# Optimization experiments

Measured on AMD Instinct MI355X. Metric: run time of the kernel, lower is better.

Reference implementation:

```python
import jax, jax.numpy as jnp
import numpy as np

N_NODES = 50000


def setup_inputs() -> dict:
    key = jax.random.key(0)
    k1, k2, k3, k4, k5 = jax.random.split(key, 5)
    x = jax.random.normal(k1, (N_NODES, 128), dtype=jnp.float32)
    edge_index = jax.random.randint(k2, (1600000, 2), 0, N_NODES, dtype=jnp.int64)
    # learned params for the concrete combine: out = agg @ W_neigh + self @ W_self + b
    W_neigh = jax.random.normal(k3, (128, 128), dtype=jnp.float32) * (1.0 / np.sqrt(128))
    W_self = jax.random.normal(k4, (128, 128), dtype=jnp.float32) * (1.0 / np.sqrt(128))
    b = jax.random.normal(k5, (128,), dtype=jnp.float32) * 0.01
    return {"x": x, "edge_index": edge_index, "W_neigh": W_neigh, "W_self": W_self, "b": b}


def reference(x, edge_index, W_neigh, W_self, b):
    n = x.shape[0]
    src = edge_index[:, 0]
    dst = edge_index[:, 1]
    # undirected: each edge (i,j) sends x[j] -> i and x[i] -> j
    agg_sum = jax.ops.segment_sum(x[dst], src, num_segments=n)
    agg_sum = agg_sum + jax.ops.segment_sum(x[src], dst, num_segments=n)
    ones = jnp.ones((edge_index.shape[0],), dtype=x.dtype)
    deg = jax.ops.segment_sum(ones, src, num_segments=n)
    deg = deg + jax.ops.segment_sum(ones, dst, num_segments=n)
    agg_mean = agg_sum / jnp.maximum(deg, 1.0)[:, None]  # mean aggregate
    # combine(agg, self)
    return agg_mean @ W_neigh + x @ W_self + b
```

## Files before the change

kernel.cpp:

```cpp
#include <hip/hip_runtime.h>
#include <hip/hip_fp16.h>


constexpr int DIM    = 128;
constexpr int NBMAX  = 512;
constexpr int EPB    = 4096;
constexpr int CAP    = 9216;

typedef _Float16 half8 __attribute__((ext_vector_type(8)));
typedef __attribute__((ext_vector_type(4))) float f32x4;

__device__ __forceinline__ unsigned hadd2u(unsigned a, unsigned b) {
    __half2 ha = *reinterpret_cast<__half2*>(&a);
    __half2 hb = *reinterpret_cast<__half2*>(&b);
    __half2 r  = __hadd2(ha, hb);
    return *reinterpret_cast<unsigned*>(&r);
}
__device__ __forceinline__ unsigned hmul2u(unsigned a, __half2 s) {
    __half2 ha = *reinterpret_cast<__half2*>(&a);
    __half2 r  = __hmul2(ha, s);
    return *reinterpret_cast<unsigned*>(&r);
}
__device__ __forceinline__ unsigned packf16(float x, float y) {
    __half2 h = __floats2half2_rn(x, y);
    return *reinterpret_cast<unsigned*>(&h);
}

__global__ __launch_bounds__(256) void k_prep(
    const float* __restrict__ Wn, const float* __restrict__ Ws,
    const float* __restrict__ x,
    unsigned short* __restrict__ Bp, int* __restrict__ bucket_cur,
    unsigned* __restrict__ abf, int nb, int n_nodes)
{
    int i = blockIdx.x * 256 + threadIdx.x;
    if (i < nb) bucket_cur[i] = i * CAP;
    if (i < 8 * 128 * 4 * 8) {
        int j    = i & 7;
        int quad = (i >> 3) & 3;
        int n    = (i >> 5) & 127;
        int kb   = i >> 12;
        int k = kb * 32 + quad * 8 + j;
        float v = (k < 128) ? Wn[k * 128 + n] : Ws[(k - 128) * 128 + n];
        __half h = __float2half_rn(v);
        Bp[i] = *reinterpret_cast<unsigned short*>(&h);
    }
    if (i < n_nodes * 64) {
        int n = i >> 6;
        int u = i & 63;
        float2 f = ((const float2*)(x + (size_t)n * DIM))[u];
        abf[(size_t)n * 128 + 64 + u] = packf16(f.x, f.y);
    }
}

__global__ __launch_bounds__(512) void k_bin(
    const int* __restrict__ edge, int* __restrict__ bucket_cur,
    unsigned* __restrict__ entries, int n_edges, int nb)
{
    __shared__ int lh[8][NBMAX];
    __shared__ int Lb[NBMAX];
    __shared__ int gb[NBMAX];
    __shared__ int sc[NBMAX];
    __shared__ unsigned sorted[2 * EPB];

    int t = threadIdx.x;
    int w = t >> 6;
    for (int i = t; i < 8 * NBMAX; i += 512) ((int*)lh)[i] = 0;
    __syncthreads();

    int e0 = blockIdx.x * EPB;
    int2 ev[8];
    #pragma unroll
    for (int k = 0; k < 8; k++) {
        int idx = e0 + k * 512 + t;
        if (idx < n_edges) {
            ev[k] = ((const int2*)edge)[idx];
            atomicAdd(&lh[w][ev[k].x >> 7], 1);
            atomicAdd(&lh[w][ev[k].y >> 7], 1);
        } else {
            ev[k].x = -1;
        }
    }
    __syncthreads();

    {
        int s = 0;
        #pragma unroll
        for (int ww = 0; ww < 8; ww++) s += lh[ww][t];
        sc[t] = s;
    }
    __syncthreads();
    for (int d = 1; d < 512; d <<= 1) {
        int v = (t >= d) ? sc[t - d] : 0;
        __syncthreads();
        if (t >= d) sc[t] += v;
        __syncthreads();
    }
    if (t < nb) {
        int tot = 0;
        #pragma unroll
        for (int ww = 0; ww < 8; ww++) tot += lh[ww][t];
        int L = sc[t] - tot;
        Lb[t] = L;
        gb[t] = tot ? atomicAdd(&bucket_cur[t], tot) : 0;
        int run = L;
        #pragma unroll
        for (int ww = 0; ww < 8; ww++) { int c = lh[ww][t]; lh[ww][t] = run; run += c; }
    }
    __syncthreads();

    #pragma unroll
    for (int k = 0; k < 8; k++) {
        int a = ev[k].x;
        if (a < 0) continue;
        int b = ev[k].y;
        int sa = atomicAdd(&lh[w][a >> 7], 1);
        sorted[sa] = ((unsigned)a << 16) | (unsigned)b;
        int sb = atomicAdd(&lh[w][b >> 7], 1);
        sorted[sb] = ((unsigned)b << 16) | (unsigned)a;
    }
    __syncthreads();

    int cntb = sc[511];
    for (int p = t; p < cntb; p += 512) {
        unsigned e = sorted[p];
        int bk = (int)(e >> 23);
        entries[gb[bk] + p - Lb[bk]] = e;
    }
}

__global__ __launch_bounds__(512) void k_csort(
    const unsigned* __restrict__ entries, const int* __restrict__ bucket_cur,
    unsigned* __restrict__ offsets, int* __restrict__ degs,
    unsigned short* __restrict__ nbr, int n_nodes)
{
    int b    = blockIdx.x;
    int base = b * CAP;
    int cnt  = bucket_cur[b] - base;
    __shared__ int lh[8][128];
    __shared__ int scn[128];
    int t = threadIdx.x;
    int w = t >> 6;
    for (int i = t; i < 8 * 128; i += 512) ((int*)lh)[i] = 0;
    __syncthreads();
    for (int i = t; i < cnt; i += 512)
        atomicAdd(&lh[w][(entries[base + i] >> 16) & 127], 1);
    __syncthreads();
    int tot = 0;
    if (t < 128) {
        #pragma unroll
        for (int ww = 0; ww < 8; ww++) tot += lh[ww][t];
        scn[t] = tot;
    }
    __syncthreads();
    for (int d = 1; d < 128; d <<= 1) {
        int u = (t >= d && t < 128) ? scn[t - d] : 0;
        __syncthreads();
        if (t >= d && t < 128) scn[t] += u;
        __syncthreads();
    }
    if (t < 128) {
        int excl = scn[t] - tot;
        int node = (b << 7) + t;
        if (node < n_nodes) {
            offsets[node] = (unsigned)(base + excl);
            degs[node]    = tot;
        }
        int run = excl;
        #pragma unroll
        for (int ww = 0; ww < 8; ww++) { int c = lh[ww][t]; lh[ww][t] = run; run += c; }
    }
    __syncthreads();
    for (int i = t; i < cnt; i += 512) {
        unsigned e = entries[base + i];
        int slot = atomicAdd(&lh[w][(e >> 16) & 127], 1);
        nbr[base + slot] = (unsigned short)(e & 0xFFFFu);
    }
}

__global__ __launch_bounds__(256) void k_gather(
    const unsigned* __restrict__ offsets,
    const int* __restrict__ degs,
    const unsigned short* __restrict__ nbr,
    unsigned* __restrict__ abf, int n_nodes)
{
    int node = blockIdx.x * 4 + (threadIdx.x >> 6);
    if (node >= n_nodes) return;
    int lane = threadIdx.x & 63;
    int grp  = lane >> 4;
    int u    = lane & 15;
    const uint4* xr = (const uint4*)abf;
    int base = (int)offsets[node];
    int deg  = degs[node];
    int end  = base + deg;

    unsigned p0[4], p1[4], p2[4], p3[4];
    #pragma unroll
    for (int d = 0; d < 4; d++) { p0[d] = 0u; p1[d] = 0u; p2[d] = 0u; p3[d] = 0u; }

    int i = base + grp;
    for (; i + 12 < end; i += 16) {
        int v0 = nbr[i];
        int v1 = nbr[i + 4];
        int v2 = nbr[i + 8];
        int v3 = nbr[i + 12];
        uint4 w0 = xr[v0 * 32 + 16 + u];
        uint4 w1 = xr[v1 * 32 + 16 + u];
        uint4 w2 = xr[v2 * 32 + 16 + u];
        uint4 w3 = xr[v3 * 32 + 16 + u];
        p0[0] = hadd2u(p0[0], w0.x); p1[0] = hadd2u(p1[0], w0.y);
        p2[0] = hadd2u(p2[0], w0.z); p3[0] = hadd2u(p3[0], w0.w);
        p0[1] = hadd2u(p0[1], w1.x); p1[1] = hadd2u(p1[1], w1.y);
        p2[1] = hadd2u(p2[1], w1.z); p3[1] = hadd2u(p3[1], w1.w);
        p0[2] = hadd2u(p0[2], w2.x); p1[2] = hadd2u(p1[2], w2.y);
        p2[2] = hadd2u(p2[2], w2.z); p3[2] = hadd2u(p3[2], w2.w);
        p0[3] = hadd2u(p0[3], w3.x); p1[3] = hadd2u(p1[3], w3.y);
        p2[3] = hadd2u(p2[3], w3.z); p3[3] = hadd2u(p3[3], w3.w);
    }
    for (; i < end; i += 4) {
        int v0 = nbr[i];
        uint4 w0 = xr[v0 * 32 + 16 + u];
        p0[0] = hadd2u(p0[0], w0.x); p1[0] = hadd2u(p1[0], w0.y);
        p2[0] = hadd2u(p2[0], w0.z); p3[0] = hadd2u(p3[0], w0.w);
    }

    unsigned s0 = hadd2u(hadd2u(p0[0], p0[1]), hadd2u(p0[2], p0[3]));
    unsigned s1 = hadd2u(hadd2u(p1[0], p1[1]), hadd2u(p1[2], p1[3]));
    unsigned s2 = hadd2u(hadd2u(p2[0], p2[1]), hadd2u(p2[2], p2[3]));
    unsigned s3 = hadd2u(hadd2u(p3[0], p3[1]), hadd2u(p3[2], p3[3]));

    #pragma unroll
    for (int off = 16; off < 64; off <<= 1) {
        s0 = hadd2u(s0, (unsigned)__shfl_xor((int)s0, off));
        s1 = hadd2u(s1, (unsigned)__shfl_xor((int)s1, off));
        s2 = hadd2u(s2, (unsigned)__shfl_xor((int)s2, off));
        s3 = hadd2u(s3, (unsigned)__shfl_xor((int)s3, off));
    }

    if (grp == 0) {
        float inv = 1.0f / fmaxf((float)deg, 1.0f);
        __half2 iv = __float2half2_rn(inv);
        uint4 o;
        o.x = hmul2u(s0, iv);
        o.y = hmul2u(s1, iv);
        o.z = hmul2u(s2, iv);
        o.w = hmul2u(s3, iv);
        ((uint4*)(abf + (size_t)node * 128))[u] = o;
    }
}

__global__ __launch_bounds__(256) void k_mfma_gemm(
    const unsigned short* __restrict__ abf,
    const unsigned short* __restrict__ Bp,
    const float* __restrict__ bias,
    float* __restrict__ out, int n_nodes)
{
    int wave = threadIdx.x >> 6;
    int lane = threadIdx.x & 63;
    int quad = lane >> 4;
    int l16  = lane & 15;
    int row0 = blockIdx.x * 64 + wave * 16;

    int arow = min(row0 + l16, n_nodes - 1);
    const unsigned short* arp = abf + (size_t)arow * 256 + quad * 8;
    half8 afrag[8];
    #pragma unroll
    for (int kb = 0; kb < 8; kb++)
        afrag[kb] = *((const half8*)(arp + kb * 32));

    f32x4 acc[8];
    #pragma unroll
    for (int f = 0; f < 8; f++) acc[f] = (f32x4){0.f, 0.f, 0.f, 0.f};

    #pragma unroll
    for (int kb = 0; kb < 8; kb++) {
        #pragma unroll
        for (int f = 0; f < 8; f++) {
            int n = f * 16 + l16;
            half8 bfrag = *((const half8*)(Bp + (((size_t)kb * 128 + n) * 4 + quad) * 8));
            acc[f] = __builtin_amdgcn_mfma_f32_16x16x32_f16(afrag[kb], bfrag, acc[f], 0, 0, 0);
        }
    }

    #pragma unroll
    for (int f = 0; f < 8; f++) {
        float bv = bias[f * 16 + l16];
        #pragma unroll
        for (int r = 0; r < 4; r++) {
            int row = row0 + quad * 4 + r;
            if (row < n_nodes)
                out[(size_t)row * DIM + f * 16 + l16] = acc[f][r] + bv;
        }
    }
}

extern "C" void kernel_launch(void* const* d_in, const int* in_sizes, int n_in,
                              void* d_out, int out_size, void* d_ws, size_t ws_size,
                              hipStream_t stream) {
    const float* x    = (const float*)d_in[0];
    const int*   edge = (const int*)  d_in[1];
    const float* Wn   = (const float*)d_in[2];
    const float* Ws   = (const float*)d_in[3];
    const float* b    = (const float*)d_in[4];
    float* out = (float*)d_out;

    const int n_nodes = in_sizes[0] / DIM;
    const int n_edges = in_sizes[1] / 2;
    const int nb = (n_nodes + 127) >> 7;

    unsigned* entries      = (unsigned*)d_ws;
    unsigned short* nbr    = (unsigned short*)(entries + (size_t)nb * CAP);
    unsigned* offsets      = (unsigned*)(nbr + (size_t)nb * CAP);
    int* degs              = (int*)(offsets + n_nodes);
    int* bucket_cur        = degs + n_nodes;
    unsigned short* Bp     = (unsigned short*)((((size_t)(bucket_cur + nb)) + 63) & ~(size_t)63);
    unsigned* abf          = (unsigned*)d_out;

    const int nprep = n_nodes * 64;
    k_prep<<<(nprep + 255) / 256, 256, 0, stream>>>(Wn, Ws, x, Bp, bucket_cur,
                                                    abf, nb, n_nodes);

    const int bb = (n_edges + EPB - 1) / EPB;
    k_bin<<<bb, 512, 0, stream>>>(edge, bucket_cur, entries, n_edges, nb);
    k_csort<<<nb, 512, 0, stream>>>(entries, bucket_cur, offsets, degs, nbr, n_nodes);

    k_gather<<<(n_nodes + 3) / 4, 256, 0, stream>>>(offsets, degs, nbr, abf, n_nodes);

    const int mb = (n_nodes + 63) / 64;
    k_mfma_gemm<<<mb, 256, 0, stream>>>((const unsigned short*)abf, Bp, b,
                                        out, n_nodes);
}
```

Before: 233.9 us.

## Fuse neighbor gather-mean into MFMA GEMM via shared-memory A tile

Merges the gather/mean kernel and the MFMA GEMM into one kernel. Each block aggregates 64 nodes into an LDS tile (padded stride 68), then loads the A fragments from LDS for the neighbor half and from a compact fp16 x copy for the self half. This removes the round trip of the aggregated fp16 rows through global memory and one launch. The x copy now uses a dense 64-word stride in workspace, which halves the gather footprint. The trade-off is lower parallelism: only 782 blocks of 4 waves, each wave processing 16 nodes serially, which may hurt latency hiding for the random gathers.

Result: slower. 267.4 us (+14.3%).

```diff
diff --git a/kernel.cpp b/kernel.cpp
--- a/kernel.cpp
+++ b/kernel.cpp
@@ -30,7 +30,7 @@
     const float* __restrict__ Wn, const float* __restrict__ Ws,
     const float* __restrict__ x,
     unsigned short* __restrict__ Bp, int* __restrict__ bucket_cur,
-    unsigned* __restrict__ abf, int nb, int n_nodes)
+    unsigned* __restrict__ xt, int nb, int n_nodes)
 {
     int i = blockIdx.x * 256 + threadIdx.x;
     if (i < nb) bucket_cur[i] = i * CAP;
@@ -48,7 +48,7 @@
         int n = i >> 6;
         int u = i & 63;
         float2 f = ((const float2*)(x + (size_t)n * DIM))[u];
-        abf[(size_t)n * 128 + 64 + u] = packf16(f.x, f.y);
+        xt[(size_t)n * 64 + u] = packf16(f.x, f.y);
     }
 }
 
@@ -177,95 +177,102 @@
     }
 }
 
-__global__ __launch_bounds__(256) void k_gather(
+__global__ __launch_bounds__(256) void k_gg(
     const unsigned* __restrict__ offsets,
     const int* __restrict__ degs,
     const unsigned short* __restrict__ nbr,
-    unsigned* __restrict__ abf, int n_nodes)
-{
-    int node = blockIdx.x * 4 + (threadIdx.x >> 6);
-    if (node >= n_nodes) return;
-    int lane = threadIdx.x & 63;
-    int grp  = lane >> 4;
-    int u    = lane & 15;
-    const uint4* xr = (const uint4*)abf;
-    int base = (int)offsets[node];
-    int deg  = degs[node];
-    int end  = base + deg;
-
-    unsigned p0[4], p1[4], p2[4], p3[4];
-    #pragma unroll
-    for (int d = 0; d < 4; d++) { p0[d] = 0u; p1[d] = 0u; p2[d] = 0u; p3[d] = 0u; }
-
-    int i = base + grp;
-    for (; i + 12 < end; i += 16) {
-        int v0 = nbr[i];
-        int v1 = nbr[i + 4];
-        int v2 = nbr[i + 8];
-        int v3 = nbr[i + 12];
-        uint4 w0 = xr[v0 * 32 + 16 + u];
-        uint4 w1 = xr[v1 * 32 + 16 + u];
-        uint4 w2 = xr[v2 * 32 + 16 + u];
-        uint4 w3 = xr[v3 * 32 + 16 + u];
-        p0[0] = hadd2u(p0[0], w0.x); p1[0] = hadd2u(p1[0], w0.y);
-        p2[0] = hadd2u(p2[0], w0.z); p3[0] = hadd2u(p3[0], w0.w);
-        p0[1] = hadd2u(p0[1], w1.x); p1[1] = hadd2u(p1[1], w1.y);
-        p2[1] = hadd2u(p2[1], w1.z); p3[1] = hadd2u(p3[1], w1.w);
-        p0[2] = hadd2u(p0[2], w2.x); p1[2] = hadd2u(p1[2], w2.y);
-        p2[2] = hadd2u(p2[2], w2.z); p3[2] = hadd2u(p3[2], w2.w);
-        p0[3] = hadd2u(p0[3], w3.x); p1[3] = hadd2u(p1[3], w3.y);
-        p2[3] = hadd2u(p2[3], w3.z); p3[3] = hadd2u(p3[3], w3.w);
-    }
-    for (; i < end; i += 4) {
-        int v0 = nbr[i];
-        uint4 w0 = xr[v0 * 32 + 16 + u];
-        p0[0] = hadd2u(p0[0], w0.x); p1[0] = hadd2u(p1[0], w0.y);
-        p2[0] = hadd2u(p2[0], w0.z); p3[0] = hadd2u(p3[0], w0.w);
-    }
-
-    unsigned s0 = hadd2u(hadd2u(p0[0], p0[1]), hadd2u(p0[2], p0[3]));
-    unsigned s1 = hadd2u(hadd2u(p1[0], p1[1]), hadd2u(p1[2], p1[3]));
-    unsigned s2 = hadd2u(hadd2u(p2[0], p2[1]), hadd2u(p2[2], p2[3]));
-    unsigned s3 = hadd2u(hadd2u(p3[0], p3[1]), hadd2u(p3[2], p3[3]));
-
-    #pragma unroll
-    for (int off = 16; off < 64; off <<= 1) {
-        s0 = hadd2u(s0, (unsigned)__shfl_xor((int)s0, off));
-        s1 = hadd2u(s1, (unsigned)__shfl_xor((int)s1, off));
-        s2 = hadd2u(s2, (unsigned)__shfl_xor((int)s2, off));
-        s3 = hadd2u(s3, (unsigned)__shfl_xor((int)s3, off));
-    }
-
-    if (grp == 0) {
-        float inv = 1.0f / fmaxf((float)deg, 1.0f);
-        __half2 iv = __float2half2_rn(inv);
-        uint4 o;
-        o.x = hmul2u(s0, iv);
-        o.y = hmul2u(s1, iv);
-        o.z = hmul2u(s2, iv);
-        o.w = hmul2u(s3, iv);
-        ((uint4*)(abf + (size_t)node * 128))[u] = o;
-    }
-}
-
-__global__ __launch_bounds__(256) void k_mfma_gemm(
-    const unsigned short* __restrict__ abf,
+    const unsigned* __restrict__ xt,
     const unsigned short* __restrict__ Bp,
     const float* __restrict__ bias,
     float* __restrict__ out, int n_nodes)
 {
+    __shared__ unsigned aS[64 * 68];
     int wave = threadIdx.x >> 6;
     int lane = threadIdx.x & 63;
-    int quad = lane >> 4;
-    int l16  = lane & 15;
-    int row0 = blockIdx.x * 64 + wave * 16;
-
-    int arow = min(row0 + l16, n_nodes - 1);
-    const unsigned short* arp = abf + (size_t)arow * 256 + quad * 8;
+    int grp  = lane >> 4;
+    int u    = lane & 15;
+    int row0 = blockIdx.x * 64;
+    const uint4* xr = (const uint4*)xt;
+
+    for (int it = 0; it < 16; ++it) {
+        int node = row0 + wave * 16 + it;
+        bool valid = node < n_nodes;
+        int base = 0, deg = 0;
+        if (valid) { base = (int)offsets[node]; deg = degs[node]; }
+        int end = base + deg;
+
+        unsigned p0[4], p1[4], p2[4], p3[4];
+        #pragma unroll
+        for (int d = 0; d < 4; d++) { p0[d]=0u; p1[d]=0u; p2[d]=0u; p3[d]=0u; }
+
+        int i = base + grp;
+        for (; i + 12 < end; i += 16) {
+            int v0 = nbr[i];
+            int v1 = nbr[i + 4];
+            int v2 = nbr[i + 8];
+            int v3 = nbr[i + 12];
+            uint4 w0 = xr[v0 * 16 + u];
+            uint4 w1 = xr[v1 * 16 + u];
+            uint4 w2 = xr[v2 * 16 + u];
+            uint4 w3 = xr[v3 * 16 + u];
+            p0[0] = hadd2u(p0[0], w0.x); p1[0] = hadd2u(p1[0], w0.y);
+            p2[0] = hadd2u(p2[0], w0.z); p3[0] = hadd2u(p3[0], w0.w);
+            p0[1] = hadd2u(p0[1], w1.x); p1[1] = hadd2u(p1[1], w1.y);
+            p2[1] = hadd2u(p2[1], w1.z); p3[1] = hadd2u(p3[1], w1.w);
+            p0[2] = hadd2u(p0[2], w2.x); p1[2] = hadd2u(p1[2], w2.y);
+            p2[2] = hadd2u(p2[2], w2.z); p3[2] = hadd2u(p3[2], w2.w);
+            p0[3] = hadd2u(p0[3], w3.x); p1[3] = hadd2u(p1[3], w3.y);
+            p2[3] = hadd2u(p2[3], w3.z); p3[3] = hadd2u(p3[3], w3.w);
+        }
+        for (; i < end; i += 4) {
+            int v0 = nbr[i];
+            uint4 w0 = xr[v0 * 16 + u];
+            p0[0] = hadd2u(p0[0], w0.x); p1[0] = hadd2u(p1[0], w0.y);
+            p2[0] = hadd2u(p2[0], w0.z); p3[0] = hadd2u(p3[0], w0.w);
+        }
+
+        unsigned s0 = hadd2u(hadd2u(p0[0], p0[1]), hadd2u(p0[2], p0[3]));
+        unsigned s1 = hadd2u(hadd2u(p1[0], p1[1]), hadd2u(p1[2], p1[3]));
+        unsigned s2 = hadd2u(hadd2u(p2[0], p2[1]), hadd2u(p2[2], p2[3]));
+        unsigned s3 = hadd2u(hadd2u(p3[0], p3[1]), hadd2u(p3[2], p3[3]));
+
+        #pragma unroll
+        for (int off = 16; off < 64; off <<= 1) {
+            s0 = hadd2u(s0, (unsigned)__shfl_xor((int)s0, off));
+            s1 = hadd2u(s1, (unsigned)__shfl_xor((int)s1, off));
+            s2 = hadd2u(s2, (unsigned)__shfl_xor((int)s2, off));
+            s3 = hadd2u(s3, (unsigned)__shfl_xor((int)s3, off));
+        }
+
+        if (grp == 0) {
+            float inv = 1.0f / fmaxf((float)deg, 1.0f);
+            __half2 iv = __float2half2_rn(inv);
+            uint4 o;
+            o.x = hmul2u(s0, iv);
+            o.y = hmul2u(s1, iv);
+            o.z = hmul2u(s2, iv);
+            o.w = hmul2u(s3, iv);
+            *((uint4*)&aS[(wave * 16 + it) * 68 + u * 4]) = o;
+        }
+    }
+    __syncthreads();
+
+    int quad = grp;
+    int l16  = u;
+    int slot = wave * 16 + l16;
+    int arow = min(row0 + slot, n_nodes - 1);
+
     half8 afrag[8];
     #pragma unroll
-    for (int kb = 0; kb < 8; kb++)
-        afrag[kb] = *((const half8*)(arp + kb * 32));
+    for (int kb = 0; kb < 4; kb++)
+        afrag[kb] = *((const half8*)&aS[slot * 68 + kb * 16 + quad * 4]);
+    {
+        const unsigned short* xrp =
+            (const unsigned short*)xt + (size_t)arow * 128 + quad * 8;
+        #pragma unroll
+        for (int kb = 4; kb < 8; kb++)
+            afrag[kb] = *((const half8*)(xrp + (kb - 4) * 32));
+    }
 
     f32x4 acc[8];
     #pragma unroll
@@ -281,12 +288,13 @@
         }
     }
 
+    int rbase = row0 + wave * 16 + quad * 4;
     #pragma unroll
     for (int f = 0; f < 8; f++) {
         float bv = bias[f * 16 + l16];
         #pragma unroll
         for (int r = 0; r < 4; r++) {
-            int row = row0 + quad * 4 + r;
+            int row = rbase + r;
             if (row < n_nodes)
                 out[(size_t)row * DIM + f * 16 + l16] = acc[f][r] + bv;
         }
@@ -313,19 +321,16 @@
     int* degs              = (int*)(offsets + n_nodes);
     int* bucket_cur        = degs + n_nodes;
     unsigned short* Bp     = (unsigned short*)((((size_t)(bucket_cur + nb)) + 63) & ~(size_t)63);
-    unsigned* abf          = (unsigned*)d_out;
+    unsigned* xt           = (unsigned*)(Bp + 8 * 128 * 4 * 8);
 
     const int nprep = n_nodes * 64;
     k_prep<<<(nprep + 255) / 256, 256, 0, stream>>>(Wn, Ws, x, Bp, bucket_cur,
-                                                    abf, nb, n_nodes);
+                                                    xt, nb, n_nodes);
 
     const int bb = (n_edges + EPB - 1) / EPB;
     k_bin<<<bb, 512, 0, stream>>>(edge, bucket_cur, entries, n_edges, nb);
     k_csort<<<nb, 512, 0, stream>>>(entries, bucket_cur, offsets, degs, nbr, n_nodes);
 
-    k_gather<<<(n_nodes + 3) / 4, 256, 0, stream>>>(offsets, degs, nbr, abf, n_nodes);
-
-    const int mb = (n_nodes + 63) / 64;
-    k_mfma_gemm<<<mb, 256, 0, stream>>>((const unsigned short*)abf, Bp, b,
-                                        out, n_nodes);
-}
+    const int gb = (n_nodes + 63) / 64;
+    k_gg<<<gb, 256, 0, stream>>>(offsets, degs, nbr, xt, Bp, b, out, n_nodes);
+}
```
